# Kernel optimization log

Hardware: AMD Instinct MI355X
Metric: run time of the kernel (lower is better)

The kernel has to match this reference:

```python
import jax, jax.numpy as jnp
import numpy as np

N_NODES = 50000
N_EDGES = 600000
D = 128


def sage_conv(x, edge_index, Wl, bl, Wr):
    # PyG SAGEConv (mean aggr): out = lin_l(mean_{j in N(i)} x_j) + lin_r(x_i)
    src, dst = edge_index[0], edge_index[1]
    msgs = x[src]  # [E, D] gather of neighbor features
    summed = jax.ops.segment_sum(msgs, dst, num_segments=N_NODES)  # [N, D]
    deg = jax.ops.segment_sum(jnp.ones((msgs.shape[0],), x.dtype), dst, num_segments=N_NODES)
    mean = summed / jnp.maximum(deg, 1.0)[:, None]
    return mean @ Wl.T + bl + x @ Wr.T


def setup_inputs() -> dict:
    key = jax.random.key(0)
    ks = jax.random.split(key, 12)
    s = 1.0 / np.sqrt(D)
    inp = {
        "x": jax.random.normal(ks[0], (N_NODES, D), dtype=jnp.float32),
        "edge_index": jax.random.randint(ks[1], (2, N_EDGES), 0, N_NODES, dtype=jnp.int64),
    }
    for i, layer in enumerate([1, 2, 3]):
        inp[f"Wl{layer}"] = jax.random.uniform(ks[2 + 3 * i], (D, D), jnp.float32, -s, s)
        inp[f"bl{layer}"] = jax.random.uniform(ks[3 + 3 * i], (D,), jnp.float32, -s, s)
        inp[f"Wr{layer}"] = jax.random.uniform(ks[4 + 3 * i], (D, D), jnp.float32, -s, s)
    return inp


def reference(x, edge_index, Wl1, bl1, Wr1, Wl2, bl2, Wr2, Wl3, bl3, Wr3):
    h = jax.nn.relu(sage_conv(x, edge_index, Wl1, bl1, Wr1))
    h = jax.nn.relu(sage_conv(h, edge_index, Wl2, bl2, Wr2))
    h = jax.nn.relu(sage_conv(h, edge_index, Wl3, bl3, Wr3))
    return h
```

## Files before the change

### kernel.cpp

```cpp
#include <hip/hip_runtime.h>
#include <hip/hip_bf16.h>
#include <stdint.h>

#define N_NODES 50000
#define N_EDGES 600000
#define DD 128
#define K2 256
#define M_PAD 50048
#define MAXDEG 64
#define NREP 4
#define SEGCAP 16
#define POISON 0xAAAAAAAAu

#define FILL_BLOCKS 2344
#define PREP_BLOCKS 3125

typedef __bf16 bf16x8 __attribute__((ext_vector_type(8)));
typedef float floatx4 __attribute__((ext_vector_type(4)));

__device__ __forceinline__ ushort f2bf(float f) {
    union { float f; uint u; } v; v.f = f;
    uint u = v.u;
    u += 0x7fffu + ((u >> 16) & 1u);
    return (ushort)(u >> 16);
}
__device__ __forceinline__ float bf2f(ushort h) {
    union { uint u; float f; } v; v.u = ((uint)h) << 16;
    return v.f;
}
__device__ __forceinline__ void accum8(float* a, uint4 p) {
    a[0] += bf2f((ushort)(p.x & 0xffffu)); a[1] += bf2f((ushort)(p.x >> 16));
    a[2] += bf2f((ushort)(p.y & 0xffffu)); a[3] += bf2f((ushort)(p.y >> 16));
    a[4] += bf2f((ushort)(p.z & 0xffffu)); a[5] += bf2f((ushort)(p.z >> 16));
    a[6] += bf2f((ushort)(p.w & 0xffffu)); a[7] += bf2f((ushort)(p.w >> 16));
}
__device__ __forceinline__ uint4 packf8(float4 f0, float4 f1) {
    uint4 o;
    o.x = (uint)f2bf(f0.x) | ((uint)f2bf(f0.y) << 16);
    o.y = (uint)f2bf(f0.z) | ((uint)f2bf(f0.w) << 16);
    o.z = (uint)f2bf(f1.x) | ((uint)f2bf(f1.y) << 16);
    o.w = (uint)f2bf(f1.z) | ((uint)f2bf(f1.w) << 16);
    return o;
}


__global__ void k_build(const float* __restrict__ x, ushort* __restrict__ X,
                        uint* __restrict__ cursor, ushort* __restrict__ col,
                        const int* __restrict__ eidx,
                        const float* __restrict__ Wl1, const float* __restrict__ Wr1,
                        const float* __restrict__ Wl2, const float* __restrict__ Wr2,
                        const float* __restrict__ Wl3, const float* __restrict__ Wr3,
                        ushort* __restrict__ Wb) {
    if (blockIdx.x < FILL_BLOCKS) {
        int t = blockIdx.x * 256 + threadIdx.x;
        if (t >= N_EDGES) return;
        int src = eidx[t];
        int dst = eidx[N_EDGES + t];
        int r = t & (NREP - 1);
        uint o = atomicAdd(&cursor[(size_t)dst * NREP + r], 1u) - POISON;
        if (o < SEGCAP) col[dst * MAXDEG + r * SEGCAP + o] = (ushort)src;
    } else {
        int idx = (blockIdx.x - FILL_BLOCKS) * 256 + threadIdx.x;
        if (idx < 3 * DD * K2 / 8) {
            int l = idx >> 12;
            int r = idx & 4095;
            int j = r >> 5, c = (r & 31) * 8;
            const float* Wl = (l == 0) ? Wl1 : (l == 1) ? Wl2 : Wl3;
            const float* Wr = (l == 0) ? Wr1 : (l == 1) ? Wr2 : Wr3;
            const float* W = (c < DD) ? &Wl[j * DD + c] : &Wr[j * DD + c - DD];
            float4 f0 = *(const float4*)W;
            float4 f1 = *(const float4*)(W + 4);
            *(uint4*)&Wb[(size_t)l * DD * K2 + j * K2 + c] = packf8(f0, f1);
        }
        if (idx >= N_NODES * 16) return;
        int i = idx >> 4, c = (idx & 15) * 8;
        float4 f0 = *(const float4*)&x[(size_t)i * DD + c];
        float4 f1 = *(const float4*)&x[(size_t)i * DD + c + 4];
        *(uint4*)&X[(size_t)i * DD + c] = packf8(f0, f1);
    }
}


template <bool LAST>
__global__ __launch_bounds__(256) void k_fused(const ushort* __restrict__ Xin,
                                               const ushort* __restrict__ Wb,
                                               const float* __restrict__ bias,
                                               const uint* __restrict__ cursor,
                                               const ushort* __restrict__ colell,
                                               ushort* __restrict__ Xout,
                                               float* __restrict__ out) {
    __shared__ ushort Ms[64 * 136];
    __shared__ ushort Bs[128 * 72];
    int tid = threadIdx.x;
    int wave = tid >> 6, lane = tid & 63;
    int quad = lane >> 4, l16 = lane & 15;
    int i0 = blockIdx.x * 64;

    uint4 xr0, xr1, xr2, xr3;
    {
        const ushort* xrow = &Xin[(size_t)(i0 + wave * 16 + l16) * DD + quad * 8];
        xr0 = *(const uint4*)&xrow[0];
        xr1 = *(const uint4*)&xrow[32];
        xr2 = *(const uint4*)&xrow[64];
        xr3 = *(const uint4*)&xrow[96];
    }

    const int choff = l16 * 8;
    #pragma unroll 2
    for (int t = 0; t < 16; ++t) {
        int node = i0 + wave * 16 + t;
        uint4 c4 = *(const uint4*)&cursor[(size_t)node * NREP];
        int d0 = (int)min(c4.x - POISON, (uint)SEGCAP);
        int d1 = (int)min(c4.y - POISON, (uint)SEGCAP);
        int d2 = (int)min(c4.z - POISON, (uint)SEGCAP);
        int d3 = (int)min(c4.w - POISON, (uint)SEGCAP);
        int deg = d0 + d1 + d2 + d3;
        int dr = (quad == 0) ? d0 : (quad == 1) ? d1 : (quad == 2) ? d2 : d3;
        int pre = ((quad > 0) ? d0 : 0) + ((quad > 1) ? d1 : 0) + ((quad > 2) ? d2 : 0);
        int nb = (int)colell[node * MAXDEG + lane];
        int dstb = ((l16 < dr) ? (pre + l16) : 63) * 4;
        nb = __builtin_amdgcn_ds_permute(dstb, nb);

        float a[8] = {0, 0, 0, 0, 0, 0, 0, 0};
        int dm1 = deg - 1;
        for (int base = 0; base < deg; base += 16) {
            int ii0 = base + quad, ii1 = ii0 + 4, ii2 = ii0 + 8, ii3 = ii0 + 12;
            int s0 = __shfl(nb, min(ii0, dm1), 64);
            int s1 = __shfl(nb, min(ii1, dm1), 64);
            int s2 = __shfl(nb, min(ii2, dm1), 64);
            int s3 = __shfl(nb, min(ii3, dm1), 64);
            uint4 p0 = *(const uint4*)&Xin[(size_t)s0 * DD + choff];
            uint4 p1 = *(const uint4*)&Xin[(size_t)s1 * DD + choff];
            uint4 p2 = *(const uint4*)&Xin[(size_t)s2 * DD + choff];
            uint4 p3 = *(const uint4*)&Xin[(size_t)s3 * DD + choff];
            if (ii0 < deg) accum8(a, p0);
            if (ii1 < deg) accum8(a, p1);
            if (ii2 < deg) accum8(a, p2);
            if (ii3 < deg) accum8(a, p3);
        }
        float inv = 1.0f / (float)max(deg, 1);
        #pragma unroll
        for (int j = 0; j < 8; ++j) {
            float v = a[j];
            v += __shfl_xor(v, 16, 64);
            v += __shfl_xor(v, 32, 64);
            a[j] = v * inv;
        }
        if (lane < 16) {
            uint4 o;
            o.x = (uint)f2bf(a[0]) | ((uint)f2bf(a[1]) << 16);
            o.y = (uint)f2bf(a[2]) | ((uint)f2bf(a[3]) << 16);
            o.z = (uint)f2bf(a[4]) | ((uint)f2bf(a[5]) << 16);
            o.w = (uint)f2bf(a[6]) | ((uint)f2bf(a[7]) << 16);
            *(uint4*)&Ms[(wave * 16 + t) * 136 + l16 * 8] = o;
        }
    }
    __syncthreads();

    floatx4 acc[8];
    #pragma unroll
    for (int ct = 0; ct < 8; ++ct) acc[ct] = (floatx4){0.f, 0.f, 0.f, 0.f};

    #pragma unroll
    for (int kbi = 0; kbi < 4; ++kbi) {
        int kb = kbi * 64;
        for (int it = 0; it < 4; ++it) {
            int idx = tid + it * 256;
            int j = idx >> 3, c = (idx & 7) * 8;
            *(uint4*)&Bs[j * 72 + c] = *(const uint4*)&Wb[j * K2 + kb + c];
        }
        __syncthreads();
        #pragma unroll
        for (int ksi = 0; ksi < 2; ++ksi) {
            int ks = ksi * 32;
            bf16x8 av;
            if (kbi < 2) {
                av = *(const bf16x8*)&Ms[(wave * 16 + l16) * 136 + kb + ks + quad * 8];
            } else {
                union { uint4 u; bf16x8 v; } cvt;
                cvt.u = (kbi == 2) ? (ksi == 0 ? xr0 : xr1)
                                   : (ksi == 0 ? xr2 : xr3);
                av = cvt.v;
            }
            #pragma unroll
            for (int ct = 0; ct < 8; ++ct) {
                bf16x8 b = *(const bf16x8*)&Bs[(ct * 16 + l16) * 72 + ks + quad * 8];
                acc[ct] = __builtin_amdgcn_mfma_f32_16x16x32_bf16(av, b, acc[ct], 0, 0, 0);
            }
        }
        __syncthreads();
    }

    #pragma unroll
    for (int ct = 0; ct < 8; ++ct) {
        int colg = ct * 16 + l16;
        float bv = bias[colg];
        #pragma unroll
        for (int r = 0; r < 4; ++r) {
            int row = i0 + wave * 16 + quad * 4 + r;
            if (row < N_NODES) {
                float v = fmaxf(acc[ct][r] + bv, 0.0f);
                if (LAST)
                    out[(size_t)row * DD + colg] = v;
                else
                    Xout[(size_t)row * DD + colg] = f2bf(v);
            }
        }
    }
}


extern "C" void kernel_launch(void* const* d_in, const int* in_sizes, int n_in,
                              void* d_out, int out_size, void* d_ws, size_t ws_size,
                              hipStream_t stream) {
    const float* x = (const float*)d_in[0];
    const int* eidx = (const int*)d_in[1];

    char* ws = (char*)d_ws;
    size_t off = 0;
    auto alloc = [&](size_t bytes) {
        void* p = ws + off;
        off += (bytes + 255) & ~(size_t)255;
        return p;
    };
    ushort* X0 = (ushort*)alloc((size_t)M_PAD * DD * 2);
    ushort* X1 = (ushort*)alloc((size_t)M_PAD * DD * 2);
    uint* cursor = (uint*)alloc((size_t)M_PAD * NREP * 4);
    ushort* col = (ushort*)alloc((size_t)M_PAD * MAXDEG * 2);
    ushort* Wb = (ushort*)alloc((size_t)3 * DD * K2 * 2);
    (void)ws_size;

    k_build<<<FILL_BLOCKS + PREP_BLOCKS, 256, 0, stream>>>(
        x, X0, cursor, col, eidx,
        (const float*)d_in[2], (const float*)d_in[4],
        (const float*)d_in[5], (const float*)d_in[7],
        (const float*)d_in[8], (const float*)d_in[10], Wb);

    const int grid = M_PAD / 64;

    k_fused<false><<<grid, 256, 0, stream>>>(
        X0, Wb, (const float*)d_in[3], cursor, col, X1, nullptr);
    k_fused<false><<<grid, 256, 0, stream>>>(
        X1, Wb + (size_t)DD * K2, (const float*)d_in[6], cursor, col, X0, nullptr);
    k_fused<true><<<grid, 256, 0, stream>>>(
        X0, Wb + (size_t)2 * DD * K2, (const float*)d_in[9], cursor, col,
        nullptr, (float*)d_out);
}
```

Baseline: 250.6 us.

## Halve rows per block, split MFMA columns across waves, prefetch neighbor lists

New measurement: 260.0 us. +3.7%, slower.

```diff
diff --git a/kernel.cpp b/kernel.cpp
--- a/kernel.cpp
+++ b/kernel.cpp
@@ -82,53 +82,64 @@
 
 
 template <bool LAST>
-__global__ __launch_bounds__(256) void k_fused(const ushort* __restrict__ Xin,
-                                               const ushort* __restrict__ Wb,
-                                               const float* __restrict__ bias,
-                                               const uint* __restrict__ cursor,
-                                               const ushort* __restrict__ colell,
-                                               ushort* __restrict__ Xout,
-                                               float* __restrict__ out) {
-    __shared__ ushort Ms[64 * 136];
+__global__ __launch_bounds__(256, 6) void k_fused(const ushort* __restrict__ Xin,
+                                                  const ushort* __restrict__ Wb,
+                                                  const float* __restrict__ bias,
+                                                  const uint* __restrict__ cursor,
+                                                  const ushort* __restrict__ colell,
+                                                  ushort* __restrict__ Xout,
+                                                  float* __restrict__ out) {
+    __shared__ ushort Ms[32 * 136];
     __shared__ ushort Bs[128 * 72];
     int tid = threadIdx.x;
     int wave = tid >> 6, lane = tid & 63;
     int quad = lane >> 4, l16 = lane & 15;
-    int i0 = blockIdx.x * 64;
+    int i0 = blockIdx.x * 32;
+    int stripe = wave & 1;
+    int chalf = wave >> 1;
 
     uint4 xr0, xr1, xr2, xr3;
     {
-        const ushort* xrow = &Xin[(size_t)(i0 + wave * 16 + l16) * DD + quad * 8];
+        const ushort* xrow = &Xin[(size_t)(i0 + stripe * 16 + l16) * DD + quad * 8];
         xr0 = *(const uint4*)&xrow[0];
         xr1 = *(const uint4*)&xrow[32];
         xr2 = *(const uint4*)&xrow[64];
         xr3 = *(const uint4*)&xrow[96];
     }
 
-    const int choff = l16 * 8;
-    #pragma unroll 2
-    for (int t = 0; t < 16; ++t) {
-        int node = i0 + wave * 16 + t;
-        uint4 c4 = *(const uint4*)&cursor[(size_t)node * NREP];
-        int d0 = (int)min(c4.x - POISON, (uint)SEGCAP);
-        int d1 = (int)min(c4.y - POISON, (uint)SEGCAP);
-        int d2 = (int)min(c4.z - POISON, (uint)SEGCAP);
-        int d3 = (int)min(c4.w - POISON, (uint)SEGCAP);
+    int n0 = i0 + wave * 8;
+    uint cw = cursor[(size_t)n0 * NREP + (lane & 31)];
+    int nbv[8];
+    #pragma unroll
+    for (int t = 0; t < 8; ++t)
+        nbv[t] = (int)colell[(n0 + t) * MAXDEG + lane];
+    int degs[8];
+    #pragma unroll
+    for (int t = 0; t < 8; ++t) {
+        int d0 = (int)min((uint)__shfl((int)cw, t * 4 + 0, 64) - POISON, (uint)SEGCAP);
+        int d1 = (int)min((uint)__shfl((int)cw, t * 4 + 1, 64) - POISON, (uint)SEGCAP);
+        int d2 = (int)min((uint)__shfl((int)cw, t * 4 + 2, 64) - POISON, (uint)SEGCAP);
+        int d3 = (int)min((uint)__shfl((int)cw, t * 4 + 3, 64) - POISON, (uint)SEGCAP);
         int deg = d0 + d1 + d2 + d3;
         int dr = (quad == 0) ? d0 : (quad == 1) ? d1 : (quad == 2) ? d2 : d3;
         int pre = ((quad > 0) ? d0 : 0) + ((quad > 1) ? d1 : 0) + ((quad > 2) ? d2 : 0);
-        int nb = (int)colell[node * MAXDEG + lane];
         int dstb = ((l16 < dr) ? (pre + l16) : 63) * 4;
-        nb = __builtin_amdgcn_ds_permute(dstb, nb);
-
+        nbv[t] = __builtin_amdgcn_ds_permute(dstb, nbv[t]);
+        degs[t] = deg;
+    }
+
+    const int choff = l16 * 8;
+    #pragma unroll
+    for (int t = 0; t < 8; ++t) {
         float a[8] = {0, 0, 0, 0, 0, 0, 0, 0};
+        int deg = degs[t];
         int dm1 = deg - 1;
         for (int base = 0; base < deg; base += 16) {
             int ii0 = base + quad, ii1 = ii0 + 4, ii2 = ii0 + 8, ii3 = ii0 + 12;
-            int s0 = __shfl(nb, min(ii0, dm1), 64);
-            int s1 = __shfl(nb, min(ii1, dm1), 64);
-            int s2 = __shfl(nb, min(ii2, dm1), 64);
-            int s3 = __shfl(nb, min(ii3, dm1), 64);
+            int s0 = __shfl(nbv[t], min(ii0, dm1), 64);
+            int s1 = __shfl(nbv[t], min(ii1, dm1), 64);
+            int s2 = __shfl(nbv[t], min(ii2, dm1), 64);
+            int s3 = __shfl(nbv[t], min(ii3, dm1), 64);
             uint4 p0 = *(const uint4*)&Xin[(size_t)s0 * DD + choff];
             uint4 p1 = *(const uint4*)&Xin[(size_t)s1 * DD + choff];
             uint4 p2 = *(const uint4*)&Xin[(size_t)s2 * DD + choff];
@@ -152,14 +163,14 @@
             o.y = (uint)f2bf(a[2]) | ((uint)f2bf(a[3]) << 16);
             o.z = (uint)f2bf(a[4]) | ((uint)f2bf(a[5]) << 16);
             o.w = (uint)f2bf(a[6]) | ((uint)f2bf(a[7]) << 16);
-            *(uint4*)&Ms[(wave * 16 + t) * 136 + l16 * 8] = o;
+            *(uint4*)&Ms[(wave * 8 + t) * 136 + l16 * 8] = o;
         }
     }
     __syncthreads();
 
-    floatx4 acc[8];
-    #pragma unroll
-    for (int ct = 0; ct < 8; ++ct) acc[ct] = (floatx4){0.f, 0.f, 0.f, 0.f};
+    floatx4 acc[4];
+    #pragma unroll
+    for (int ct = 0; ct < 4; ++ct) acc[ct] = (floatx4){0.f, 0.f, 0.f, 0.f};
 
     #pragma unroll
     for (int kbi = 0; kbi < 4; ++kbi) {
@@ -175,7 +186,7 @@
             int ks = ksi * 32;
             bf16x8 av;
             if (kbi < 2) {
-                av = *(const bf16x8*)&Ms[(wave * 16 + l16) * 136 + kb + ks + quad * 8];
+                av = *(const bf16x8*)&Ms[(stripe * 16 + l16) * 136 + kb + ks + quad * 8];
             } else {
                 union { uint4 u; bf16x8 v; } cvt;
                 cvt.u = (kbi == 2) ? (ksi == 0 ? xr0 : xr1)
@@ -183,8 +194,8 @@
                 av = cvt.v;
             }
             #pragma unroll
-            for (int ct = 0; ct < 8; ++ct) {
-                bf16x8 b = *(const bf16x8*)&Bs[(ct * 16 + l16) * 72 + ks + quad * 8];
+            for (int ct = 0; ct < 4; ++ct) {
+                bf16x8 b = *(const bf16x8*)&Bs[(chalf * 64 + ct * 16 + l16) * 72 + ks + quad * 8];
                 acc[ct] = __builtin_amdgcn_mfma_f32_16x16x32_bf16(av, b, acc[ct], 0, 0, 0);
             }
         }
@@ -192,12 +203,12 @@
     }
 
     #pragma unroll
-    for (int ct = 0; ct < 8; ++ct) {
-        int colg = ct * 16 + l16;
+    for (int ct = 0; ct < 4; ++ct) {
+        int colg = chalf * 64 + ct * 16 + l16;
         float bv = bias[colg];
         #pragma unroll
         for (int r = 0; r < 4; ++r) {
-            int row = i0 + wave * 16 + quad * 4 + r;
+            int row = i0 + stripe * 16 + quad * 4 + r;
             if (row < N_NODES) {
                 float v = fmaxf(acc[ct][r] + bv, 0.0f);
                 if (LAST)
@@ -236,7 +247,7 @@
         (const float*)d_in[5], (const float*)d_in[7],
         (const float*)d_in[8], (const float*)d_in[10], Wb);
 
-    const int grid = M_PAD / 64;
+    const int grid = M_PAD / 32;
 
     k_fused<false><<<grid, 256, 0, stream>>>(
         X0, Wb, (const float*)d_in[3], cursor, col, X1, nullptr);
```

## Batch neighbor-list loads and fully unroll aggregation loop for memory-level parallelism

Applied to the files above, without the earlier changes.

Result: slower. 289.0 us (+15.3%).

```diff
diff --git a/kernel.cpp b/kernel.cpp
--- a/kernel.cpp
+++ b/kernel.cpp
@@ -82,13 +82,13 @@
 
 
 template <bool LAST>
-__global__ __launch_bounds__(256) void k_fused(const ushort* __restrict__ Xin,
-                                               const ushort* __restrict__ Wb,
-                                               const float* __restrict__ bias,
-                                               const uint* __restrict__ cursor,
-                                               const ushort* __restrict__ colell,
-                                               ushort* __restrict__ Xout,
-                                               float* __restrict__ out) {
+__global__ __launch_bounds__(256, 4) void k_fused(const ushort* __restrict__ Xin,
+                                                  const ushort* __restrict__ Wb,
+                                                  const float* __restrict__ bias,
+                                                  const uint* __restrict__ cursor,
+                                                  const ushort* __restrict__ colell,
+                                                  ushort* __restrict__ Xout,
+                                                  float* __restrict__ out) {
     __shared__ ushort Ms[64 * 136];
     __shared__ ushort Bs[128 * 72];
     int tid = threadIdx.x;
@@ -96,39 +96,39 @@
     int quad = lane >> 4, l16 = lane & 15;
     int i0 = blockIdx.x * 64;
 
-    uint4 xr0, xr1, xr2, xr3;
-    {
-        const ushort* xrow = &Xin[(size_t)(i0 + wave * 16 + l16) * DD + quad * 8];
-        xr0 = *(const uint4*)&xrow[0];
-        xr1 = *(const uint4*)&xrow[32];
-        xr2 = *(const uint4*)&xrow[64];
-        xr3 = *(const uint4*)&xrow[96];
-    }
-
-    const int choff = l16 * 8;
-    #pragma unroll 2
+    int n0 = i0 + wave * 16;
+    uint cw = cursor[(size_t)n0 * NREP + lane];
+    int nbv[16];
+    #pragma unroll
+    for (int t = 0; t < 16; ++t)
+        nbv[t] = (int)colell[(n0 + t) * MAXDEG + lane];
+    int degs[16];
+    #pragma unroll
     for (int t = 0; t < 16; ++t) {
-        int node = i0 + wave * 16 + t;
-        uint4 c4 = *(const uint4*)&cursor[(size_t)node * NREP];
-        int d0 = (int)min(c4.x - POISON, (uint)SEGCAP);
-        int d1 = (int)min(c4.y - POISON, (uint)SEGCAP);
-        int d2 = (int)min(c4.z - POISON, (uint)SEGCAP);
-        int d3 = (int)min(c4.w - POISON, (uint)SEGCAP);
+        int d0 = (int)min((uint)__shfl((int)cw, t * 4 + 0, 64) - POISON, (uint)SEGCAP);
+        int d1 = (int)min((uint)__shfl((int)cw, t * 4 + 1, 64) - POISON, (uint)SEGCAP);
+        int d2 = (int)min((uint)__shfl((int)cw, t * 4 + 2, 64) - POISON, (uint)SEGCAP);
+        int d3 = (int)min((uint)__shfl((int)cw, t * 4 + 3, 64) - POISON, (uint)SEGCAP);
         int deg = d0 + d1 + d2 + d3;
         int dr = (quad == 0) ? d0 : (quad == 1) ? d1 : (quad == 2) ? d2 : d3;
         int pre = ((quad > 0) ? d0 : 0) + ((quad > 1) ? d1 : 0) + ((quad > 2) ? d2 : 0);
-        int nb = (int)colell[node * MAXDEG + lane];
         int dstb = ((l16 < dr) ? (pre + l16) : 63) * 4;
-        nb = __builtin_amdgcn_ds_permute(dstb, nb);
-
+        nbv[t] = __builtin_amdgcn_ds_permute(dstb, nbv[t]);
+        degs[t] = deg;
+    }
+
+    const int choff = l16 * 8;
+    #pragma unroll
+    for (int t = 0; t < 16; ++t) {
         float a[8] = {0, 0, 0, 0, 0, 0, 0, 0};
+        int deg = degs[t];
         int dm1 = deg - 1;
-        for (int base = 0; base < deg; base += 16) {
-            int ii0 = base + quad, ii1 = ii0 + 4, ii2 = ii0 + 8, ii3 = ii0 + 12;
-            int s0 = __shfl(nb, min(ii0, dm1), 64);
-            int s1 = __shfl(nb, min(ii1, dm1), 64);
-            int s2 = __shfl(nb, min(ii2, dm1), 64);
-            int s3 = __shfl(nb, min(ii3, dm1), 64);
+        {
+            int ii0 = quad, ii1 = quad + 4, ii2 = quad + 8, ii3 = quad + 12;
+            int s0 = __shfl(nbv[t], min(ii0, dm1), 64);
+            int s1 = __shfl(nbv[t], min(ii1, dm1), 64);
+            int s2 = __shfl(nbv[t], min(ii2, dm1), 64);
+            int s3 = __shfl(nbv[t], min(ii3, dm1), 64);
             uint4 p0 = *(const uint4*)&Xin[(size_t)s0 * DD + choff];
             uint4 p1 = *(const uint4*)&Xin[(size_t)s1 * DD + choff];
             uint4 p2 = *(const uint4*)&Xin[(size_t)s2 * DD + choff];
@@ -138,6 +138,23 @@
             if (ii2 < deg) accum8(a, p2);
             if (ii3 < deg) accum8(a, p3);
         }
+        if (deg > 16) {
+            for (int base = 16; base < deg; base += 16) {
+                int ii0 = base + quad, ii1 = ii0 + 4, ii2 = ii0 + 8, ii3 = ii0 + 12;
+                int s0 = __shfl(nbv[t], min(ii0, dm1), 64);
+                int s1 = __shfl(nbv[t], min(ii1, dm1), 64);
+                int s2 = __shfl(nbv[t], min(ii2, dm1), 64);
+                int s3 = __shfl(nbv[t], min(ii3, dm1), 64);
+                uint4 p0 = *(const uint4*)&Xin[(size_t)s0 * DD + choff];
+                uint4 p1 = *(const uint4*)&Xin[(size_t)s1 * DD + choff];
+                uint4 p2 = *(const uint4*)&Xin[(size_t)s2 * DD + choff];
+                uint4 p3 = *(const uint4*)&Xin[(size_t)s3 * DD + choff];
+                if (ii0 < deg) accum8(a, p0);
+                if (ii1 < deg) accum8(a, p1);
+                if (ii2 < deg) accum8(a, p2);
+                if (ii3 < deg) accum8(a, p3);
+            }
+        }
         float inv = 1.0f / (float)max(deg, 1);
         #pragma unroll
         for (int j = 0; j < 8; ++j) {
@@ -156,6 +173,15 @@
         }
     }
     __syncthreads();
+
+    uint4 xr0, xr1, xr2, xr3;
+    {
+        const ushort* xrow = &Xin[(size_t)(i0 + wave * 16 + l16) * DD + quad * 8];
+        xr0 = *(const uint4*)&xrow[0];
+        xr1 = *(const uint4*)&xrow[32];
+        xr2 = *(const uint4*)&xrow[64];
+        xr3 = *(const uint4*)&xrow[96];
+    }
 
     floatx4 acc[8];
     #pragma unroll
```
